# Kernel tuning notes

Measured on AMD Instinct MI355X. Metric: run time of the kernel, lower is better.

Reference implementation:

```python
import jax, jax.numpy as jnp
import numpy as np

LATENT_DIM = 512
IN_CH = 256
OUT_CH = 256
KSIZE = 3
BATCH = 16
RES = 128
SQRT2 = float(np.sqrt(2.0))


def setup_inputs() -> dict:
    key = jax.random.key(0)
    k1, k2, k3, k4, k5 = jax.random.split(key, 5)
    content = jax.random.normal(k1, (BATCH, IN_CH, RES, RES), dtype=jnp.float32)
    latent = jax.random.normal(k2, (BATCH, LATENT_DIM), dtype=jnp.float32)
    noise = jax.random.normal(k3, (BATCH, 1, RES, RES), dtype=jnp.float32)
    # affine: LinearLayer(latentDim, inChannels, doActivation=False), bias filled with 1
    aff_w = jax.random.normal(k4, (IN_CH, LATENT_DIM), dtype=jnp.float32)
    aff_b = jnp.ones((IN_CH,), dtype=jnp.float32)
    conv_w = jax.random.normal(k5, (OUT_CH, IN_CH, KSIZE, KSIZE), dtype=jnp.float32)
    bias = jnp.zeros((1, OUT_CH, 1, 1), dtype=jnp.float32)
    noise_weight = jnp.zeros((), dtype=jnp.float32)
    return {"content": content, "latent": latent, "noise": noise,
            "aff_w": aff_w, "aff_b": aff_b, "conv_w": conv_w,
            "bias": bias, "noise_weight": noise_weight}


def reference(content, latent, noise, aff_w, aff_b, conv_w, bias, noise_weight):
    # affine style: F.linear(latent, W * sqrt(1/latentDim)) + bias (bias init 1, lrMult 1, no act)
    w_mult = np.sqrt(1.0 / aff_w.shape[1]).astype(np.float32)
    style = latent @ (aff_w * w_mult).T + aff_b  # [B, Cin]
    # demodulation factor: d[b,o] = rsqrt(sum_{i,kh,kw} (W[o,i]*style[b,i])^2 + eps)
    w_sq = jnp.sum(conv_w * conv_w, axis=(2, 3))  # [Cout, Cin]
    demod = jax.lax.rsqrt(jnp.einsum('oi,bi->bo', w_sq, style * style) + 1e-8)  # [B, Cout]
    # modulate activations instead of weights (mathematically identical to per-sample grouped conv)
    x = content * style[:, :, None, None]
    pad = KSIZE // 2
    y = jax.lax.conv_general_dilated(
        x, conv_w, window_strides=(1, 1), padding=((pad, pad), (pad, pad)),
        dimension_numbers=('NCHW', 'OIHW', 'NCHW'))
    y = y * demod[:, :, None, None]  # [B, Cout, H, W]
    y = y + noise_weight * noise + bias
    return jax.nn.leaky_relu(y, negative_slope=0.2) * SQRT2
```

## Files before the change

### kernel.cpp

```cpp
#include <hip/hip_runtime.h>


typedef __bf16 bf16;
typedef bf16 bf16x8 __attribute__((ext_vector_type(8)));
typedef bf16 bf16x4 __attribute__((ext_vector_type(4)));
typedef float f32x4 __attribute__((ext_vector_type(4)));

#define GLOBAL_AS __attribute__((address_space(1)))
#define LDS_AS __attribute__((address_space(3)))

__global__ __launch_bounds__(256) void style_k(const float* __restrict__ latent,
                                               const float* __restrict__ aff_w,
                                               const float* __restrict__ aff_b,
                                               float* __restrict__ style) {
  const int wid = blockIdx.x * 4 + (threadIdx.x >> 6);
  const int lane = threadIdx.x & 63;
  const int b = wid >> 8, i = wid & 255;
  float acc = 0.f;
#pragma unroll
  for (int k = 0; k < 8; ++k) {
    const int l = lane + 64 * k;
    acc += latent[b * 512 + l] * aff_w[i * 512 + l];
  }
#pragma unroll
  for (int off = 32; off > 0; off >>= 1) acc += __shfl_xor(acc, off, 64);
  if (lane == 0) style[b * 256 + i] = acc * 0.04419417382415922f + aff_b[i];
}

__global__ __launch_bounds__(256) void demod_k(const float* __restrict__ conv_w,
                                               const float* __restrict__ style,
                                               float* __restrict__ demod) {
  __shared__ float s_wsq[256];
  const int o = blockIdx.x, i = threadIdx.x;
  float wsq = 0.f;
#pragma unroll
  for (int t = 0; t < 9; ++t) {
    const float w = conv_w[(o * 256 + i) * 9 + t];
    wsq += w * w;
  }
  s_wsq[i] = wsq;
  __syncthreads();
  const int wv = threadIdx.x >> 6, lane = threadIdx.x & 63;
  for (int b = wv; b < 16; b += 4) {
    float p = 0.f;
#pragma unroll
    for (int k = 0; k < 4; ++k) {
      const int ii = lane + 64 * k;
      const float s = style[b * 256 + ii];
      p += s_wsq[ii] * s * s;
    }
#pragma unroll
    for (int off = 32; off > 0; off >>= 1) p += __shfl_xor(p, off, 64);
    if (lane == 0) demod[b * 256 + o] = rsqrtf(p + 1e-8f);
  }
}

__global__ __launch_bounds__(256) void wprep_k(const float* __restrict__ conv_w,
                                               bf16* __restrict__ wp) {
  const int idx = blockIdx.x * 256 + threadIdx.x;
  const int ci = idx & 31;
  const int t3 = idx >> 5;
  const int kw = t3 % 3;
  const int t4 = t3 / 3;
  const int m = t4 & 255;
  const int t5 = t4 >> 8;
  const int cc = t5 & 7, kh = t5 >> 3;
  const float v = conv_w[((m * 256 + cc * 32 + ci) * 3 + kh) * 3 + kw];
  wp[idx] = (bf16)v;
}

__global__ __launch_bounds__(256) void conv_k(const float* __restrict__ content,
                                              const float* __restrict__ noise,
                                              const float* __restrict__ bias,
                                              const float* __restrict__ nwp,
                                              const float* __restrict__ style,
                                              const float* __restrict__ demod,
                                              const bf16* __restrict__ wp,
                                              float* __restrict__ out) {
  __shared__ __align__(16) char smem[24576 + 10400];
  bf16* ldsA = (bf16*)smem;
  bf16* ldsX = (bf16*)(smem + 24576);

  const int tid = threadIdx.x;
  const int lane = tid & 63, wv = tid >> 6;
  const int bid = blockIdx.x;
  const int mt = bid & 1;
  const int sp = bid >> 1;
  const int h = sp & 127, b = sp >> 7;
  const int g = lane >> 4, nl = lane & 15;
  const int m0 = (wv & 1) * 64, n0 = (wv >> 1) * 64;
  const int wS = tid & 127, qi = tid >> 7;

  f32x4 acc[4][4];
  const f32x4 zero4 = {0.f, 0.f, 0.f, 0.f};
#pragma unroll
  for (int mb = 0; mb < 4; ++mb)
#pragma unroll
    for (int nb = 0; nb < 4; ++nb) acc[mb][nb] = zero4;

  const float* srcb = content + ((size_t)b * 256) * 16384;

  for (int cc = 0; cc < 8; ++cc) {
    const float* stl = style + b * 256 + cc * 32;
    for (int kh = 0; kh < 3; ++kh) {
      const int gh = h + kh - 1;
      if (gh < 0 || gh >= 128) continue;
      {
        const bf16* seg = wp + ((size_t)((kh * 8 + cc) * 256 + mt * 128)) * 96;
#pragma unroll
        for (int i = 0; i < 6; ++i) {
          const int u = wv * 384 + i * 64 + lane;
          __builtin_amdgcn_global_load_lds((const GLOBAL_AS void*)(seg + u * 8),
                                           (LDS_AS void*)(ldsA + u * 8), 16, 0, 0);
        }
      }
      {
        const float* src = srcb + (size_t)(cc * 32) * 16384 + gh * 128 + wS;
#pragma unroll
        for (int jj = 0; jj < 4; ++jj) {
          const int q = qi + jj * 2;
          const float v0 = src[(q * 4 + 0) * 16384] * stl[q * 4 + 0];
          const float v1 = src[(q * 4 + 1) * 16384] * stl[q * 4 + 1];
          const float v2 = src[(q * 4 + 2) * 16384] * stl[q * 4 + 2];
          const float v3 = src[(q * 4 + 3) * 16384] * stl[q * 4 + 3];
          bf16x4 pk = {(bf16)v0, (bf16)v1, (bf16)v2, (bf16)v3};
          *(bf16x4*)(ldsX + (wS + 1) * 40 + q * 4) = pk;
        }
        if (tid < 16) {
          const int xh = (tid >> 3) ? 129 : 0;
          const int q = tid & 7;
          bf16x4 z = {(bf16)0.f, (bf16)0.f, (bf16)0.f, (bf16)0.f};
          *(bf16x4*)(ldsX + xh * 40 + q * 4) = z;
        }
      }
      __syncthreads();
#pragma unroll
      for (int kw = 0; kw < 3; ++kw) {
        bf16x8 af[4], xf[4];
#pragma unroll
        for (int mb = 0; mb < 4; ++mb)
          af[mb] = *(const bf16x8*)(ldsA + (m0 + mb * 16 + nl) * 96 + kw * 32 + g * 8);
#pragma unroll
        for (int nb = 0; nb < 4; ++nb)
          xf[nb] = *(const bf16x8*)(ldsX + (n0 + nb * 16 + nl + kw) * 40 + g * 8);
#pragma unroll
        for (int mb = 0; mb < 4; ++mb)
#pragma unroll
          for (int nb = 0; nb < 4; ++nb)
            acc[mb][nb] =
                __builtin_amdgcn_mfma_f32_16x16x32_bf16(af[mb], xf[nb], acc[mb][nb], 0, 0, 0);
      }
      __syncthreads();
    }
  }

  const float nw = nwp[0];
#pragma unroll
  for (int mb = 0; mb < 4; ++mb) {
    const int o = mt * 128 + m0 + mb * 16 + g * 4;
    const f32x4 dm = *(const f32x4*)(demod + b * 256 + o);
    const f32x4 bs = *(const f32x4*)(bias + o);
#pragma unroll
    for (int nb = 0; nb < 4; ++nb) {
      const int wo = n0 + nb * 16 + nl;
      const float nz = nw * noise[b * 16384 + h * 128 + wo];
      float* op = out + ((size_t)(b * 256 + o)) * 16384 + h * 128 + wo;
#pragma unroll
      for (int r = 0; r < 4; ++r) {
        float y = acc[mb][nb][r] * dm[r] + nz + bs[r];
        y = (y > 0.f ? y : 0.2f * y) * 1.41421356237f;
        op[(size_t)r * 16384] = y;
      }
    }
  }
}

extern "C" void kernel_launch(void* const* d_in, const int* in_sizes, int n_in,
                              void* d_out, int out_size, void* d_ws, size_t ws_size,
                              hipStream_t stream) {
  const float* content = (const float*)d_in[0];
  const float* latent = (const float*)d_in[1];
  const float* noise = (const float*)d_in[2];
  const float* aff_w = (const float*)d_in[3];
  const float* aff_b = (const float*)d_in[4];
  const float* conv_w = (const float*)d_in[5];
  const float* bias = (const float*)d_in[6];
  const float* nw = (const float*)d_in[7];
  float* out = (float*)d_out;

  float* style = (float*)d_ws;
  float* demod = style + 4096;
  bf16* wp = (bf16*)((char*)d_ws + 32768);

  style_k<<<1024, 256, 0, stream>>>(latent, aff_w, aff_b, style);
  demod_k<<<256, 256, 0, stream>>>(conv_w, style, demod);
  wprep_k<<<2304, 256, 0, stream>>>(conv_w, wp);
  conv_k<<<4096, 256, 0, stream>>>(content, noise, bias, nw, style, demod, wp, out);
}
```

Baseline: 724.0 us.

## Pre-transpose modulated activations to padded NHWC bf16 and drop LDS staging in conv

Adds a separate pass that multiplies content by style, converts it to bf16 and writes a zero-padded channel-last buffer in workspace. The weights are also repacked into a fragment-friendly order. A new conv kernel then reads both operands for each MFMA straight from global memory, with no LDS and no barriers, and the block index is remapped to improve cache locality. This removes the strided per-channel fp32 loads and repeated conversion done inside the conv, at the cost of an extra write and read of a large intermediate and reliance on L2 for reuse. The old path is kept as a fallback when the workspace is too small.

```diff
diff --git a/kernel.cpp b/kernel.cpp
--- a/kernel.cpp
+++ b/kernel.cpp
@@ -54,6 +54,135 @@
     if (lane == 0) demod[b * 256 + o] = rsqrtf(p + 1e-8f);
   }
 }
+
+
+__global__ __launch_bounds__(256) void wprep2_k(const float* __restrict__ conv_w,
+                                                bf16* __restrict__ wp) {
+  const int idx = blockIdx.x * 256 + threadIdx.x;
+  const int ci8 = idx & 7;
+  const int m = (idx >> 3) & 255;
+  const int g = (idx >> 11) & 3;
+  const int r = idx >> 13;
+  const int kw = r % 3;
+  const int r2 = r / 3;
+  const int kh = r2 % 3;
+  const int cc = r2 / 3;
+  const int c = cc * 32 + g * 8 + ci8;
+  wp[idx] = (bf16)conv_w[((m * 256 + c) * 3 + kh) * 3 + kw];
+}
+
+__global__ __launch_bounds__(256) void xprep_k(const float* __restrict__ content,
+                                               const float* __restrict__ style,
+                                               bf16* __restrict__ Xp) {
+  __shared__ float T[128 * 65];
+  const int tid = threadIdx.x;
+  const int cchunk = blockIdx.x & 3;
+  const int h = (blockIdx.x >> 2) & 127;
+  const int b = blockIdx.x >> 9;
+
+  const int w = tid & 127, half = tid >> 7;
+  const float* src = content + ((size_t)(b * 256 + cchunk * 64) * 128 + h) * 128;
+  const float* stl = style + b * 256 + cchunk * 64;
+#pragma unroll
+  for (int iter = 0; iter < 32; ++iter) {
+    const int cl = iter * 2 + half;
+    T[w * 65 + cl] = src[(size_t)cl * 16384 + w] * stl[cl];
+  }
+  __syncthreads();
+
+  bf16* rowb = Xp + ((size_t)(b * 128 + h) * 130) * 256 + cchunk * 64;
+#pragma unroll
+  for (int iter = 0; iter < 4; ++iter) {
+    const int u = iter * 256 + tid;
+    const int x = (u >> 3) + 1;
+    const int p = u & 7;
+    const float* tr = &T[(x - 1) * 65 + p * 8];
+    bf16x8 pk = {(bf16)tr[0], (bf16)tr[1], (bf16)tr[2], (bf16)tr[3],
+                 (bf16)tr[4], (bf16)tr[5], (bf16)tr[6], (bf16)tr[7]};
+    *(bf16x8*)(rowb + (size_t)x * 256 + p * 8) = pk;
+  }
+  if (tid < 16) {
+    const int x = (tid >> 3) ? 129 : 0;
+    const int p = tid & 7;
+    bf16x8 z = {(bf16)0.f, (bf16)0.f, (bf16)0.f, (bf16)0.f,
+                (bf16)0.f, (bf16)0.f, (bf16)0.f, (bf16)0.f};
+    *(bf16x8*)(rowb + (size_t)x * 256 + p * 8) = z;
+  }
+}
+
+__global__ __launch_bounds__(256) void conv2_k(const bf16* __restrict__ Xp,
+                                               const bf16* __restrict__ wp,
+                                               const float* __restrict__ noise,
+                                               const float* __restrict__ bias,
+                                               const float* __restrict__ nwp,
+                                               const float* __restrict__ demod,
+                                               float* __restrict__ out) {
+  const int tid = threadIdx.x;
+  const int lane = tid & 63, wv = tid >> 6;
+  const int g = lane >> 4, nl = lane & 15;
+  const int m0 = (wv & 1) * 64, n0 = (wv >> 1) * 64;
+  const int wid = (blockIdx.x >> 3) | ((blockIdx.x & 7) << 9);
+  const int mt = wid & 1;
+  const int sp = wid >> 1;
+  const int h = sp & 127, b = sp >> 7;
+
+  f32x4 acc[4][4];
+  const f32x4 zero4 = {0.f, 0.f, 0.f, 0.f};
+#pragma unroll
+  for (int mb = 0; mb < 4; ++mb)
+#pragma unroll
+    for (int nb = 0; nb < 4; ++nb) acc[mb][nb] = zero4;
+
+  const bf16* xb = Xp + (size_t)(b * 128) * 130 * 256;
+
+  for (int cc = 0; cc < 8; ++cc) {
+    const bf16* wcc = wp + (size_t)cc * 73728;
+#pragma unroll
+    for (int kh = 0; kh < 3; ++kh) {
+      const int gh = h + kh - 1;
+      if (gh < 0 || gh >= 128) continue;
+      const bf16* xr = xb + (size_t)gh * 130 * 256 + cc * 32;
+      const bf16* wr = wcc + kh * 24576;
+#pragma unroll
+      for (int kw = 0; kw < 3; ++kw) {
+        bf16x8 af[4], xf[4];
+        const bf16* wkw = wr + kw * 8192 + g * 2048 + (mt * 128 + m0 + nl) * 8;
+#pragma unroll
+        for (int mb = 0; mb < 4; ++mb) af[mb] = *(const bf16x8*)(wkw + mb * 128);
+        const bf16* xkw = xr + (size_t)(n0 + nl + kw) * 256 + g * 8;
+#pragma unroll
+        for (int nb = 0; nb < 4; ++nb) xf[nb] = *(const bf16x8*)(xkw + (size_t)nb * 4096);
+#pragma unroll
+        for (int mb = 0; mb < 4; ++mb)
+#pragma unroll
+          for (int nb = 0; nb < 4; ++nb)
+            acc[mb][nb] =
+                __builtin_amdgcn_mfma_f32_16x16x32_bf16(af[mb], xf[nb], acc[mb][nb], 0, 0, 0);
+      }
+    }
+  }
+
+  const float nw = nwp[0];
+#pragma unroll
+  for (int mb = 0; mb < 4; ++mb) {
+    const int o = mt * 128 + m0 + mb * 16 + g * 4;
+    const f32x4 dm = *(const f32x4*)(demod + b * 256 + o);
+    const f32x4 bs = *(const f32x4*)(bias + o);
+#pragma unroll
+    for (int nb = 0; nb < 4; ++nb) {
+      const int wo = n0 + nb * 16 + nl;
+      const float nz = nw * noise[b * 16384 + h * 128 + wo];
+      float* op = out + ((size_t)(b * 256 + o)) * 16384 + h * 128 + wo;
+#pragma unroll
+      for (int r = 0; r < 4; ++r) {
+        float y = acc[mb][nb][r] * dm[r] + nz + bs[r];
+        y = (y > 0.f ? y : 0.2f * y) * 1.41421356237f;
+        op[(size_t)r * 16384] = y;
+      }
+    }
+  }
+}
+
 
 __global__ __launch_bounds__(256) void wprep_k(const float* __restrict__ conv_w,
                                                bf16* __restrict__ wp) {
@@ -192,8 +321,19 @@
   float* demod = style + 4096;
   bf16* wp = (bf16*)((char*)d_ws + 32768);
 
+  const size_t XP_OFF = 2u << 20;
+  const size_t XP_BYTES = (size_t)16 * 128 * 130 * 256 * 2;
+  bf16* Xp = (bf16*)((char*)d_ws + XP_OFF);
+
   style_k<<<1024, 256, 0, stream>>>(latent, aff_w, aff_b, style);
   demod_k<<<256, 256, 0, stream>>>(conv_w, style, demod);
-  wprep_k<<<2304, 256, 0, stream>>>(conv_w, wp);
-  conv_k<<<4096, 256, 0, stream>>>(content, noise, bias, nw, style, demod, wp, out);
-}
+
+  if (ws_size >= XP_OFF + XP_BYTES) {
+    wprep2_k<<<2304, 256, 0, stream>>>(conv_w, wp);
+    xprep_k<<<8192, 256, 0, stream>>>(content, style, Xp);
+    conv2_k<<<4096, 256, 0, stream>>>(Xp, wp, noise, bias, nw, demod, out);
+  } else {
+    wprep_k<<<2304, 256, 0, stream>>>(conv_w, wp);
+    conv_k<<<4096, 256, 0, stream>>>(content, noise, bias, nw, style, demod, wp, out);
+  }
+}
```

Measured after the change: 1.137 ms. 1.57x slower.
